# Optimization experiments

Measured on AMD Instinct MI355X. Metric: run time of the kernel, lower is better.

Reference implementation:

```python
import jax, jax.numpy as jnp
import numpy as np

N_NODES = 10000
N_EDGES = 160000
K = 25          # Chebyshev order
H = 12          # temporal filter length == time axis of x
G1 = 32         # conv output channels
NUM_CLASSES = 10
BATCH = 32


def setup_inputs() -> dict:
    key = jax.random.key(0)
    k0, k1, k2, k3 = jax.random.split(key, 4)
    x = jax.random.normal(k0, (BATCH, N_NODES, H), dtype=jnp.float32)
    edge_index = jax.random.randint(k1, (2, N_EDGES), 0, N_NODES, dtype=jnp.int32)
    conv_w = jax.random.normal(k2, (K, H, 1, G1), dtype=jnp.float32) * (1.0 / np.sqrt(K * H))
    conv_b = jnp.zeros((G1,), dtype=jnp.float32)
    fc_w = jax.random.normal(k3, (NUM_CLASSES, N_NODES * G1), dtype=jnp.float32) * 0.01
    fc_b = jnp.zeros((NUM_CLASSES,), dtype=jnp.float32)
    return {"x": x, "edge_index": edge_index, "conv_w": conv_w,
            "conv_b": conv_b, "fc_w": fc_w, "fc_b": fc_b}


def _forward(x, edge_index, conv_w, conv_b, fc_w, fc_b):
    B, N, T = x.shape
    # real part of FFT along time axis (axis=2), as in the torch forward
    xf = jnp.real(jnp.fft.fft(x, axis=2)).astype(x.dtype)  # [B, N, H]

    row, col = edge_index[0], edge_index[1]
    ones = jnp.ones(row.shape, xf.dtype)
    deg = jax.ops.segment_sum(ones, row, num_segments=N)
    dinv = jnp.where(deg > 0, deg ** -0.5, 0.0)
    # rescaled Laplacian (lmax=2): L~ = L - I = -D^{-1/2} A D^{-1/2}
    norm = -dinv[row] * dinv[col]  # [E]

    def prop(z):  # z: [B, N, H] -> L~ z
        msg = z[:, col, :] * norm[None, :, None]                       # [B, E, H]
        agg = jax.ops.segment_sum(msg.swapaxes(0, 1), row,
                                  num_segments=N)                      # [N, B, H]
        return agg.swapaxes(0, 1)                                      # [B, N, H]

    # Chebyshev recursion: Tx_0 = x, Tx_1 = L~ x, Tx_k = 2 L~ Tx_{k-1} - Tx_{k-2}
    tx_prev = xf
    out = jnp.einsum('bnh,hf->bnf', tx_prev, conv_w[0, :, 0, :])
    tx_cur = prop(tx_prev)
    out = out + jnp.einsum('bnh,hf->bnf', tx_cur, conv_w[1, :, 0, :])
    for k in range(2, K):
        tx_next = 2.0 * prop(tx_cur) - tx_prev
        out = out + jnp.einsum('bnh,hf->bnf', tx_next, conv_w[k, :, 0, :])
        tx_prev, tx_cur = tx_cur, tx_next
    out = out + conv_b                                                 # [B, N, G1]

    h = jax.nn.relu(out).reshape(B, -1)                                # [B, N*G1]
    logits = h @ fc_w.T + fc_b                                         # [B, 10]
    return jax.nn.log_softmax(logits, axis=1)


def reference(x, edge_index, conv_w, conv_b, fc_w, fc_b):
    return _forward(x, edge_index, conv_w, conv_b, fc_w, fc_b)
```

## Files before the change

kernel.cpp:

```cpp
#include <hip/hip_runtime.h>
#include <math.h>

#define N_NODES 10000
#define N_EDGES 160000
#define BATCH 32
#define HLEN 12
#define KORD 25
#define G1 32
#define NCLS 10
#define BH 384
#define BG 1024
#define NQ 8
#define QW 48
#define QU 24
#define RU 192
#define FC1_BLOCKS 313
#define EIN_BLOCKS 2500
#define RED1_BLOCKS 10
#define WPK_N (KORD * 192)

typedef unsigned int uint32;
typedef unsigned short ushort16;
typedef __attribute__((ext_vector_type(8))) short short8v;
typedef __attribute__((ext_vector_type(4))) float f32x4;
typedef __attribute__((ext_vector_type(2))) unsigned int uint2v;

struct U3 { uint32 x, y, z; };

__device__ __forceinline__ float bf16lo(uint32 u) { return __uint_as_float(u << 16); }
__device__ __forceinline__ float bf16hi(uint32 u) { return __uint_as_float(u & 0xffff0000u); }
__device__ __forceinline__ uint32 pack_bf16(float a, float b) {
    uint32 ua = __float_as_uint(a), ub = __float_as_uint(b);
    ua = (ua + 0x7fffu + ((ua >> 16) & 1u)) >> 16;
    ub = (ub + 0x7fffu + ((ub >> 16) & 1u)) & 0xffff0000u;
    return ua | ub;
}
__device__ __forceinline__ ushort16 f2bf(float a) {
    uint32 ua = __float_as_uint(a);
    return (ushort16)((ua + 0x7fffu + ((ua >> 16) & 1u)) >> 16);
}

__global__ void deg_kernel(const int* __restrict__ row, int* __restrict__ cnt) {
    int e = blockIdx.x * 256 + threadIdx.x;
    if (e < N_EDGES) atomicAdd(&cnt[row[e]], 1);
}

__global__ void dinv_kernel(const int* __restrict__ cnt, float* __restrict__ dinv) {
    int n = blockIdx.x * 256 + threadIdx.x;
    if (n < N_NODES) {
        int d = cnt[n];
        dinv[n] = (d > 0) ? 1.0f / sqrtf((float)d) : 0.0f;
    }
}

__global__ __launch_bounds__(1024) void scan_kernel(const int* __restrict__ cnt,
                                                    int* __restrict__ rowstart) {
    __shared__ int sums[1024];
    int t = threadIdx.x;
    const int per = 10;
    int base = t * per;
    int s = 0;
    for (int i = 0; i < per; i++) { int idx = base + i; if (idx < N_NODES) s += cnt[idx]; }
    sums[t] = s;
    __syncthreads();
    for (int off = 1; off < 1024; off <<= 1) {
        int v = 0;
        if (t >= off) v = sums[t - off];
        __syncthreads();
        sums[t] += v;
        __syncthreads();
    }
    int run = sums[t] - s;
    for (int i = 0; i < per; i++) {
        int idx = base + i;
        if (idx < N_NODES) { rowstart[idx] = run; run += cnt[idx]; }
    }
    if (t == 1023) rowstart[N_NODES] = run;
}

__global__ void scatter_kernel(const int* __restrict__ row, const int* __restrict__ col,
                               const float* __restrict__ dinv,
                               const int* __restrict__ rowstart, int* __restrict__ cursor,
                               int2* __restrict__ csr_pack) {
    int e = blockIdx.x * 256 + threadIdx.x;
    if (e < N_EDGES) {
        int r = row[e], c = col[e];
        int p = rowstart[r] + atomicAdd(&cursor[r], 1);
        float nrm = -dinv[r] * dinv[c];
        csr_pack[p] = make_int2(c, __float_as_int(nrm));
    }
}

__global__ void wpack_kernel(const float* __restrict__ conv_w, uint32* __restrict__ w_pk) {
    int idx = blockIdx.x * 256 + threadIdx.x;
    if (idx >= WPK_N) return;
    int k = idx / 192;
    int r = idx % 192;
    int g = r >> 6;
    int j2 = (r >> 5) & 1;
    int f = r & 31;
    int h0 = 4 * g + 2 * j2;
    float a = conv_w[(size_t)k * BH + h0 * G1 + f];
    float b = conv_w[(size_t)k * BH + (h0 + 1) * G1 + f];
    w_pk[idx] = pack_bf16(a, b);
}

__global__ __launch_bounds__(256) void fft_full_kernel(const float* __restrict__ x,
                                                       uint32* __restrict__ T0) {
    __shared__ float C[HLEN][HLEN];
    int t = threadIdx.x;
    if (t < HLEN * HLEN) {
        int k = t / HLEN, tt = t % HLEN;
        C[k][tt] = cosf(0.52359877559829887308f * (float)(k * tt));
    }
    __syncthreads();
    int tid = blockIdx.x * 256 + t;
    if (tid >= N_NODES * BATCH) return;
    int n = tid >> 5, b = tid & 31;
    const float* xp = x + (size_t)b * (N_NODES * HLEN) + (size_t)n * HLEN;
    float xr[HLEN];
#pragma unroll
    for (int i = 0; i < HLEN; i++) xr[i] = xp[i];
    float s[HLEN];
#pragma unroll
    for (int k = 0; k < HLEN; k++) {
        float acc = 0.f;
#pragma unroll
        for (int i = 0; i < HLEN; i++) acc += xr[i] * C[k][i];
        s[k] = acc;
    }
    uint32* o = T0 + (size_t)n * RU + b * 6;
#pragma unroll
    for (int j = 0; j < 6; j++) o[j] = pack_bf16(s[2 * j], s[2 * j + 1]);
}

__global__ __launch_bounds__(256) void spmm_full_kernel(
    const uint32* __restrict__ zcur, const uint32* __restrict__ zprev,
    uint32* __restrict__ znext,
    const int* __restrict__ rowstart, const int2* __restrict__ csr_pack,
    float alpha, float beta) {
    int t = threadIdx.x;
    int wv = t >> 6, l = t & 63;
    int node = blockIdx.x * 4 + wv;
    int lo3 = 3 * l;

    float a0 = 0.f, a1 = 0.f, a2 = 0.f, a3 = 0.f, a4 = 0.f, a5 = 0.f;
    int e0 = rowstart[node], e1 = rowstart[node + 1];
    int e = e0;
    if ((e & 1) && e < e1) {
        int2 p = csr_pack[e];
        float nrm = __int_as_float(p.y);
        U3 u = *(const U3*)(zcur + p.x * RU + lo3);
        a0 += nrm * bf16lo(u.x); a1 += nrm * bf16hi(u.x);
        a2 += nrm * bf16lo(u.y); a3 += nrm * bf16hi(u.y);
        a4 += nrm * bf16lo(u.z); a5 += nrm * bf16hi(u.z);
        e++;
    }
    const int4* csr4 = (const int4*)csr_pack;
    int npair = (e1 - e) >> 1;
    int base = e >> 1;
    int nch = npair >> 1;
    if (nch > 0) {
        int4 c0 = csr4[base], c1 = csr4[base + 1];
        for (int ch = 0; ch < nch; ch++) {
            int4 p0 = c0, p1 = c1;
            if (ch + 1 < nch) {
                c0 = csr4[base + 2 * ch + 2];
                c1 = csr4[base + 2 * ch + 3];
            }
            U3 uA = *(const U3*)(zcur + p0.x * RU + lo3);
            U3 uB = *(const U3*)(zcur + p0.z * RU + lo3);
            U3 uC = *(const U3*)(zcur + p1.x * RU + lo3);
            U3 uD = *(const U3*)(zcur + p1.z * RU + lo3);
            float nA = __int_as_float(p0.y), nB = __int_as_float(p0.w);
            float nC = __int_as_float(p1.y), nD = __int_as_float(p1.w);
            a0 += nA * bf16lo(uA.x) + nB * bf16lo(uB.x) + nC * bf16lo(uC.x) + nD * bf16lo(uD.x);
            a1 += nA * bf16hi(uA.x) + nB * bf16hi(uB.x) + nC * bf16hi(uC.x) + nD * bf16hi(uD.x);
            a2 += nA * bf16lo(uA.y) + nB * bf16lo(uB.y) + nC * bf16lo(uC.y) + nD * bf16lo(uD.y);
            a3 += nA * bf16hi(uA.y) + nB * bf16hi(uB.y) + nC * bf16hi(uC.y) + nD * bf16hi(uD.y);
            a4 += nA * bf16lo(uA.z) + nB * bf16lo(uB.z) + nC * bf16lo(uC.z) + nD * bf16lo(uD.z);
            a5 += nA * bf16hi(uA.z) + nB * bf16hi(uB.z) + nC * bf16hi(uC.z) + nD * bf16hi(uD.z);
        }
        e += nch * 4;
    }
    for (; e + 2 <= e1; e += 2) {
        int4 p = csr4[e >> 1];
        U3 uA = *(const U3*)(zcur + p.x * RU + lo3);
        U3 uB = *(const U3*)(zcur + p.z * RU + lo3);
        float nA = __int_as_float(p.y), nB = __int_as_float(p.w);
        a0 += nA * bf16lo(uA.x) + nB * bf16lo(uB.x);
        a1 += nA * bf16hi(uA.x) + nB * bf16hi(uB.x);
        a2 += nA * bf16lo(uA.y) + nB * bf16lo(uB.y);
        a3 += nA * bf16hi(uA.y) + nB * bf16hi(uB.y);
        a4 += nA * bf16lo(uA.z) + nB * bf16lo(uB.z);
        a5 += nA * bf16hi(uA.z) + nB * bf16hi(uB.z);
    }
    if (e < e1) {
        int2 p = csr_pack[e];
        float nrm = __int_as_float(p.y);
        U3 u = *(const U3*)(zcur + p.x * RU + lo3);
        a0 += nrm * bf16lo(u.x); a1 += nrm * bf16hi(u.x);
        a2 += nrm * bf16lo(u.y); a3 += nrm * bf16hi(u.y);
        a4 += nrm * bf16lo(u.z); a5 += nrm * bf16hi(u.z);
    }
    int idx = node * RU + lo3;
    U3 pu = *(const U3*)(zprev + idx);
    U3 ov;
    ov.x = pack_bf16(alpha * a0 - beta * bf16lo(pu.x), alpha * a1 - beta * bf16hi(pu.x));
    ov.y = pack_bf16(alpha * a2 - beta * bf16lo(pu.y), alpha * a3 - beta * bf16hi(pu.y));
    ov.z = pack_bf16(alpha * a4 - beta * bf16lo(pu.z), alpha * a5 - beta * bf16hi(pu.z));
    *(U3*)(znext + idx) = ov;
}

__global__ __launch_bounds__(256) void einfc_mfma_kernel(
    const uint32* __restrict__ T_all,
    const uint32* __restrict__ w_pk,
    const float* __restrict__ conv_b,
    const float* __restrict__ fc_w,
    float* __restrict__ partials) {
    __shared__ float lgacc[BATCH * NCLS];
    int t = threadIdx.x;
    for (int i = t; i < BATCH * NCLS; i += 256) lgacc[i] = 0.f;
    __syncthreads();
    int wv = t >> 6, l = t & 63;
    int node = blockIdx.x * 4 + wv;
    int g = l >> 4;
    int m = l & 15;
    bool gz = (g == 3);

    f32x4 acc00 = {0.f, 0.f, 0.f, 0.f};
    f32x4 acc01 = {0.f, 0.f, 0.f, 0.f};
    f32x4 acc10 = {0.f, 0.f, 0.f, 0.f};
    f32x4 acc11 = {0.f, 0.f, 0.f, 0.f};

    size_t aoff0 = (size_t)m * 6 + 2 * g;
    size_t aoff1 = (size_t)(m + 16) * 6 + 2 * g;

#pragma unroll
    for (int k = 0; k < KORD; k++) {
        const uint32* row = T_all + ((size_t)k * N_NODES + node) * RU;
        uint2v a0 = {0, 0}, a1 = {0, 0};
        uint32 b0u0 = 0, b0u1 = 0, b1u0 = 0, b1u1 = 0;
        if (!gz) {
            a0 = __builtin_nontemporal_load((const uint2v*)(row + aoff0));
            a1 = __builtin_nontemporal_load((const uint2v*)(row + aoff1));
            const uint32* wp = w_pk + (k * 3 + g) * 64 + m;
            b0u0 = wp[0];  b0u1 = wp[32];
            b1u0 = wp[16]; b1u1 = wp[48];
        }
        union { short8v v; uint32 u[4]; } A0, A1, B0, B1;
        A0.u[0] = a0.x; A0.u[1] = a0.y; A0.u[2] = 0; A0.u[3] = 0;
        A1.u[0] = a1.x; A1.u[1] = a1.y; A1.u[2] = 0; A1.u[3] = 0;
        B0.u[0] = b0u0; B0.u[1] = b0u1; B0.u[2] = 0; B0.u[3] = 0;
        B1.u[0] = b1u0; B1.u[1] = b1u1; B1.u[2] = 0; B1.u[3] = 0;
        acc00 = __builtin_amdgcn_mfma_f32_16x16x32_bf16(A0.v, B0.v, acc00, 0, 0, 0);
        acc01 = __builtin_amdgcn_mfma_f32_16x16x32_bf16(A0.v, B1.v, acc01, 0, 0, 0);
        acc10 = __builtin_amdgcn_mfma_f32_16x16x32_bf16(A1.v, B0.v, acc10, 0, 0, 0);
        acc11 = __builtin_amdgcn_mfma_f32_16x16x32_bf16(A1.v, B1.v, acc11, 0, 0, 0);
    }

    float cb0 = conv_b[m];
    float cb1 = conv_b[m + 16];
    float fw0[NCLS], fw1[NCLS];
#pragma unroll
    for (int c = 0; c < NCLS; c++) {
        const float* fp = fc_w + (size_t)c * (N_NODES * G1) + (size_t)node * G1;
        fw0[c] = fp[m];
        fw1[c] = fp[m + 16];
    }
#pragma unroll
    for (int bi = 0; bi < 2; bi++) {
        f32x4 aF = bi ? acc10 : acc00;
        f32x4 aS = bi ? acc11 : acc01;
#pragma unroll
        for (int reg = 0; reg < 4; reg++) {
            float h0 = fmaxf(aF[reg] + cb0, 0.f);
            float h1 = fmaxf(aS[reg] + cb1, 0.f);
            int b = bi * 16 + 4 * g + reg;
#pragma unroll
            for (int c = 0; c < NCLS; c++) {
                float sc = h0 * fw0[c] + h1 * fw1[c];
                sc += __shfl_xor(sc, 1);
                sc += __shfl_xor(sc, 2);
                sc += __shfl_xor(sc, 4);
                sc += __shfl_xor(sc, 8);
                if (m == 0) atomicAdd(&lgacc[b * NCLS + c], sc);
            }
        }
    }
    __syncthreads();
    for (int i = t; i < BATCH * NCLS; i += 256)
        partials[(size_t)blockIdx.x * (BATCH * NCLS) + i] = lgacc[i];
}

__global__ __launch_bounds__(320) void red1_kernel(const float* __restrict__ partials,
                                                   float* __restrict__ red) {
    int t = threadIdx.x;
    int j = blockIdx.x;
    int i0 = j * (EIN_BLOCKS / RED1_BLOCKS);
    int i1 = i0 + (EIN_BLOCKS / RED1_BLOCKS);
    float s0 = 0.f, s1 = 0.f, s2 = 0.f, s3 = 0.f;
    int i = i0;
    for (; i + 4 <= i1; i += 4) {
        s0 += partials[(size_t)(i + 0) * (BATCH * NCLS) + t];
        s1 += partials[(size_t)(i + 1) * (BATCH * NCLS) + t];
        s2 += partials[(size_t)(i + 2) * (BATCH * NCLS) + t];
        s3 += partials[(size_t)(i + 3) * (BATCH * NCLS) + t];
    }
    for (; i < i1; i++) s0 += partials[(size_t)i * (BATCH * NCLS) + t];
    red[(size_t)j * (BATCH * NCLS) + t] = s0 + s1 + s2 + s3;
}

__global__ __launch_bounds__(256) void fft_slice_kernel(const float* __restrict__ x,
                                                        ushort16* __restrict__ xf) {
    __shared__ float C[HLEN][HLEN];
    int t = threadIdx.x;
    if (t < HLEN * HLEN) {
        int k = t / HLEN, tt = t % HLEN;
        C[k][tt] = cosf(0.52359877559829887308f * (float)(k * tt));
    }
    __syncthreads();
    int tid = blockIdx.x * 256 + t;
    if (tid >= N_NODES * BATCH) return;
    int n = tid >> 5, b = tid & 31;
    const float* xp = x + (size_t)b * (N_NODES * HLEN) + (size_t)n * HLEN;
    float xr[HLEN];
#pragma unroll
    for (int i = 0; i < HLEN; i++) xr[i] = xp[i];
    int q = b >> 2, bl = b & 3;
    ushort16* o = xf + ((size_t)q * N_NODES + n) * QW + bl * HLEN;
#pragma unroll
    for (int k = 0; k < HLEN; k++) {
        float s = 0.f;
#pragma unroll
        for (int i = 0; i < HLEN; i++) s += xr[i] * C[k][i];
        o[k] = f2bf(s);
    }
}

__global__ __launch_bounds__(256) void k0_split_kernel(const uint32* __restrict__ z,
                                                       float* __restrict__ out,
                                                       const float* __restrict__ w0) {
    __shared__ float zs[4][QW];
    __shared__ float wk[HLEN * G1];
    int t = threadIdx.x;
    int wv = t >> 6, lane = t & 63;
    int bid = blockIdx.x;
    int q = bid & 7;
    int node = (bid >> 3) * 4 + wv;
    for (int i = t; i < HLEN * G1; i += 256) wk[i] = w0[i];
    if (lane < QU) {
        uint32 u = z[((size_t)q * N_NODES + node) * QU + lane];
        zs[wv][2 * lane]     = bf16lo(u);
        zs[wv][2 * lane + 1] = bf16hi(u);
    }
    __syncthreads();
    float* op = out + (size_t)node * BG + q * 128;
#pragma unroll
    for (int r = 0; r < 2; r++) {
        int j = lane + 64 * r;
        int bl = j >> 5, f = j & 31;
        const float* zb = &zs[wv][bl * HLEN];
        float s = 0.f;
#pragma unroll
        for (int h = 0; h < HLEN; h++) s += zb[h] * wk[h * G1 + f];
        op[j] = s;
    }
}

__global__ __launch_bounds__(256) void spmm_fused_kernel(
    const uint32* __restrict__ zcur, const uint32* __restrict__ zprev,
    uint32* __restrict__ znext, float* __restrict__ out,
    const int* __restrict__ rowstart, const int2* __restrict__ csr_pack,
    const float* __restrict__ wkg, float alpha, float beta) {
    __shared__ float zs[4][QW];
    __shared__ float wk[HLEN * G1];
    int t = threadIdx.x;
    int wv = t >> 6, lane = t & 63;
    int bid = blockIdx.x;
    int q = bid & 7;
    int node = (bid >> 3) * 4 + wv;
    for (int i = t; i < HLEN * G1; i += 256) wk[i] = wkg[i];

    const uint32* zq = zcur + (size_t)q * ((size_t)N_NODES * QU);
    int g  = (lane >= 24) ? 1 : 0;
    int li = lane - g * 24;
    float a0 = 0.f, a1 = 0.f;
    int e0 = rowstart[node], e1 = rowstart[node + 1];
    if (lane < 48) {
        int e = e0;
        if ((e & 1) && e < e1) {
            if (g == 0) {
                int2 p = csr_pack[e];
                float nrm = __int_as_float(p.y);
                uint32 u = zq[p.x * QU + li];
                a0 += nrm * bf16lo(u);
                a1 += nrm * bf16hi(u);
            }
            e++;
        }
        const int4* csr4 = (const int4*)csr_pack;
        int npair = (e1 - e) >> 1;
        int base = e >> 1;
        int nchunk = npair >> 2;
        if (nchunk > 0) {
            int4 c0 = csr4[base];
            int4 c1 = csr4[base + 1];
            int4 c2 = csr4[base + 2];
            int4 c3 = csr4[base + 3];
            for (int ch = 0; ch < nchunk; ch++) {
                int4 p0 = c0, p1 = c1, p2 = c2, p3 = c3;
                if (ch + 1 < nchunk) {
                    int b2 = base + (ch + 1) * 4;
                    c0 = csr4[b2];
                    c1 = csr4[b2 + 1];
                    c2 = csr4[b2 + 2];
                    c3 = csr4[b2 + 3];
                }
                int col0 = g ? p0.z : p0.x;  float n0 = __int_as_float(g ? p0.w : p0.y);
                int col1 = g ? p1.z : p1.x;  float n1 = __int_as_float(g ? p1.w : p1.y);
                int col2 = g ? p2.z : p2.x;  float n2 = __int_as_float(g ? p2.w : p2.y);
                int col3 = g ? p3.z : p3.x;  float n3 = __int_as_float(g ? p3.w : p3.y);
                uint32 u0 = zq[col0 * QU + li];
                uint32 u1 = zq[col1 * QU + li];
                uint32 u2 = zq[col2 * QU + li];
                uint32 u3 = zq[col3 * QU + li];
                a0 += n0 * bf16lo(u0) + n1 * bf16lo(u1);
                a1 += n0 * bf16hi(u0) + n1 * bf16hi(u1);
                a0 += n2 * bf16lo(u2) + n3 * bf16lo(u3);
                a1 += n2 * bf16hi(u2) + n3 * bf16hi(u3);
            }
            e += nchunk * 8;
        }
        for (; e + 2 <= e1; e += 2) {
            int4 p = csr4[e >> 1];
            int col = g ? p.z : p.x;
            float nrm = __int_as_float(g ? p.w : p.y);
            uint32 u = zq[col * QU + li];
            a0 += nrm * bf16lo(u);
            a1 += nrm * bf16hi(u);
        }
        if (e < e1 && g == 0) {
            int2 p = csr_pack[e];
            float nrm = __int_as_float(p.y);
            uint32 u = zq[p.x * QU + li];
            a0 += nrm * bf16lo(u);
            a1 += nrm * bf16hi(u);
        }
    }
    float o0 = __shfl(a0, li + 24);
    float o1 = __shfl(a1, li + 24);
    if (lane < 24) {
        a0 += o0;
        a1 += o1;
        int idx = (q * N_NODES + node) * QU + li;
        uint32 pu = zprev[idx];
        float v0 = alpha * a0 - beta * bf16lo(pu);
        float v1 = alpha * a1 - beta * bf16hi(pu);
        znext[idx] = pack_bf16(v0, v1);
        zs[wv][2 * li]     = v0;
        zs[wv][2 * li + 1] = v1;
    }
    __syncthreads();
    float* op = out + (size_t)node * BG + q * 128;
#pragma unroll
    for (int r = 0; r < 2; r++) {
        int j = lane + 64 * r;
        int bl = j >> 5, f = j & 31;
        const float* zb = &zs[wv][bl * HLEN];
        float s = 0.f;
#pragma unroll
        for (int h = 0; h < HLEN; h++) s += zb[h] * wk[h * G1 + f];
        op[j] += s;
    }
}

__global__ __launch_bounds__(256) void fc1_kernel(const float* __restrict__ out,
                                                  const float* __restrict__ conv_b,
                                                  const float* __restrict__ fc_w,
                                                  float* __restrict__ partials) {
    int t = threadIdx.x;
    int b = t >> 3;
    int sq = t & 7;
    int f0 = sq * 4;
    float4 cb4 = *(const float4*)(conv_b + f0);

    int n0 = blockIdx.x * 32;
    int n1 = n0 + 32;
    if (n1 > N_NODES) n1 = N_NODES;

    float acc[NCLS];
#pragma unroll
    for (int c = 0; c < NCLS; c++) acc[c] = 0.f;

    for (int n = n0; n < n1; n++) {
        float4 o = *(const float4*)(out + (size_t)n * BG + b * G1 + f0);
        o.x += cb4.x; o.y += cb4.y; o.z += cb4.z; o.w += cb4.w;
        o.x = o.x > 0.f ? o.x : 0.f;
        o.y = o.y > 0.f ? o.y : 0.f;
        o.z = o.z > 0.f ? o.z : 0.f;
        o.w = o.w > 0.f ? o.w : 0.f;
        const float* wp = fc_w + (size_t)n * G1 + f0;
#pragma unroll
        for (int c = 0; c < NCLS; c++) {
            float4 w = *(const float4*)(wp + (size_t)c * (N_NODES * G1));
            acc[c] += o.x * w.x + o.y * w.y + o.z * w.z + o.w * w.w;
        }
    }
#pragma unroll
    for (int c = 0; c < NCLS; c++) {
        float v = acc[c];
        v += __shfl_xor(v, 1);
        v += __shfl_xor(v, 2);
        v += __shfl_xor(v, 4);
        if (sq == 0) partials[(size_t)blockIdx.x * (BATCH * NCLS) + b * NCLS + c] = v;
    }
}

__global__ __launch_bounds__(320) void fc2_kernel(const float* __restrict__ partials,
                                                  const float* __restrict__ fc_b,
                                                  float* __restrict__ outp, int nblocks) {
    __shared__ float lg[BATCH][NCLS];
    int t = threadIdx.x;
    int b = t / NCLS, c = t % NCLS;
    float a0 = 0.f, a1 = 0.f, a2 = 0.f, a3 = 0.f;
    int i = 0;
    for (; i + 4 <= nblocks; i += 4) {
        a0 += partials[(size_t)(i + 0) * (BATCH * NCLS) + t];
        a1 += partials[(size_t)(i + 1) * (BATCH * NCLS) + t];
        a2 += partials[(size_t)(i + 2) * (BATCH * NCLS) + t];
        a3 += partials[(size_t)(i + 3) * (BATCH * NCLS) + t];
    }
    for (; i < nblocks; i++) a0 += partials[(size_t)i * (BATCH * NCLS) + t];
    lg[b][c] = a0 + a1 + a2 + a3 + fc_b[c];
    __syncthreads();
    if (t < BATCH) {
        float v[NCLS];
        float m = -1e30f;
#pragma unroll
        for (int cc = 0; cc < NCLS; cc++) { v[cc] = lg[t][cc]; m = fmaxf(m, v[cc]); }
        float s = 0.f;
#pragma unroll
        for (int cc = 0; cc < NCLS; cc++) s += expf(v[cc] - m);
        float ls = logf(s);
#pragma unroll
        for (int cc = 0; cc < NCLS; cc++) outp[t * NCLS + cc] = v[cc] - m - ls;
    }
}

extern "C" void kernel_launch(void* const* d_in, const int* in_sizes, int n_in,
                              void* d_out, int out_size, void* d_ws, size_t ws_size,
                              hipStream_t stream) {
    const float* x      = (const float*)d_in[0];
    const int*   ei     = (const int*)d_in[1];
    const float* conv_w = (const float*)d_in[2];
    const float* conv_b = (const float*)d_in[3];
    const float* fc_w   = (const float*)d_in[4];
    const float* fc_b   = (const float*)d_in[5];
    float* outp = (float*)d_out;

    const int* row = ei;
    const int* col = ei + N_EDGES;

    const size_t SLAB_U = (size_t)N_NODES * RU;

    char* ws = (char*)d_ws;
    size_t off = 0;
    auto alloc = [&](size_t bytes) -> void* {
        void* p = ws + off;
        off = (off + bytes + 255) & ~(size_t)255;
        return p;
    };
    int*    cnt      = (int*)alloc(sizeof(int) * N_NODES);
    float*  dinv     = (float*)alloc(sizeof(float) * N_NODES);
    int*    rowstart = (int*)alloc(sizeof(int) * (N_NODES + 1));
    int*    cursor   = (int*)alloc(sizeof(int) * N_NODES);
    int2*   csr_pack = (int2*)alloc(sizeof(int2) * N_EDGES);
    uint32* w_pk     = (uint32*)alloc(sizeof(uint32) * WPK_N);
    float*  partials = (float*)alloc(sizeof(float) * EIN_BLOCKS * BATCH * NCLS);
    float*  red      = (float*)cnt;

    const size_t T_ALL_BYTES = sizeof(uint32) * SLAB_U * KORD;
    bool big = (ws_size > off && (ws_size - off) >= T_ALL_BYTES + 65536);

    hipMemsetAsync(cnt, 0, sizeof(int) * N_NODES, stream);
    hipMemsetAsync(cursor, 0, sizeof(int) * N_NODES, stream);

    deg_kernel<<<(N_EDGES + 255) / 256, 256, 0, stream>>>(row, cnt);
    dinv_kernel<<<(N_NODES + 255) / 256, 256, 0, stream>>>(cnt, dinv);
    scan_kernel<<<1, 1024, 0, stream>>>(cnt, rowstart);
    scatter_kernel<<<(N_EDGES + 255) / 256, 256, 0, stream>>>(row, col, dinv, rowstart,
                                                              cursor, csr_pack);

    if (big) {
        uint32* T_all = (uint32*)alloc(T_ALL_BYTES);
        wpack_kernel<<<(WPK_N + 255) / 256, 256, 0, stream>>>(conv_w, w_pk);
        fft_full_kernel<<<(N_NODES * BATCH + 255) / 256, 256, 0, stream>>>(x, T_all);
        spmm_full_kernel<<<N_NODES / 4, 256, 0, stream>>>(T_all, T_all, T_all + SLAB_U,
                                                          rowstart, csr_pack, 1.0f, 0.0f);
        for (int k = 2; k < KORD; k++) {
            spmm_full_kernel<<<N_NODES / 4, 256, 0, stream>>>(
                T_all + SLAB_U * (size_t)(k - 1), T_all + SLAB_U * (size_t)(k - 2),
                T_all + SLAB_U * (size_t)k, rowstart, csr_pack, 2.0f, 1.0f);
        }
        einfc_mfma_kernel<<<EIN_BLOCKS, 256, 0, stream>>>(T_all, w_pk, conv_b, fc_w,
                                                          partials);
        red1_kernel<<<RED1_BLOCKS, 320, 0, stream>>>(partials, red);
        fc2_kernel<<<1, 320, 0, stream>>>(red, fc_b, outp, RED1_BLOCKS);
    } else {
        float*  outacc = (float*)alloc(sizeof(float) * (size_t)N_NODES * BG);
        uint32* slabA  = (uint32*)alloc(sizeof(uint32) * SLAB_U);
        uint32* slabB  = (uint32*)alloc(sizeof(uint32) * SLAB_U);
        const int GRID = (N_NODES / 4) * NQ;

        fft_slice_kernel<<<(N_NODES * BATCH + 255) / 256, 256, 0, stream>>>(
            x, (ushort16*)slabA);
        k0_split_kernel<<<GRID, 256, 0, stream>>>(slabA, outacc, conv_w);
        spmm_fused_kernel<<<GRID, 256, 0, stream>>>(slabA, slabA, slabB, outacc,
                                                    rowstart, csr_pack, conv_w + 1 * BH,
                                                    1.0f, 0.0f);
        uint32* zprev = slabA;
        uint32* zcur  = slabB;
        for (int k = 2; k < KORD; k++) {
            spmm_fused_kernel<<<GRID, 256, 0, stream>>>(zcur, zprev, zprev, outacc,
                                                        rowstart, csr_pack,
                                                        conv_w + (size_t)k * BH,
                                                        2.0f, 1.0f);
            uint32* tmp = zprev; zprev = zcur; zcur = tmp;
        }
        fc1_kernel<<<FC1_BLOCKS, 256, 0, stream>>>(outacc, conv_b, fc_w, partials);
        fc2_kernel<<<1, 320, 0, stream>>>(partials, fc_b, outp, FC1_BLOCKS);
    }
}
```

Before: 545.8 us.

## Partition CSR rows by column half and stage conv weights in LDS

```diff
diff --git a/kernel.cpp b/kernel.cpp
--- a/kernel.cpp
+++ b/kernel.cpp
@@ -3,6 +3,7 @@
 
 #define N_NODES 10000
 #define N_EDGES 160000
+#define HALF_N 5000
 #define BATCH 32
 #define HLEN 12
 #define KORD 25
@@ -18,6 +19,9 @@
 #define EIN_BLOCKS 2500
 #define RED1_BLOCKS 10
 #define WPK_N (KORD * 192)
+#define WCHUNKS (KORD * 3)
+#define WSTRIDE 80
+#define WLDS_N (WCHUNKS * WSTRIDE)
 
 typedef unsigned int uint32;
 typedef unsigned short ushort16;
@@ -40,9 +44,13 @@
     return (ushort16)((ua + 0x7fffu + ((ua >> 16) & 1u)) >> 16);
 }
 
-__global__ void deg_kernel(const int* __restrict__ row, int* __restrict__ cnt) {
+__global__ void deg_kernel(const int* __restrict__ row, const int* __restrict__ col,
+                           int* __restrict__ cnt, int* __restrict__ cnt0) {
     int e = blockIdx.x * 256 + threadIdx.x;
-    if (e < N_EDGES) atomicAdd(&cnt[row[e]], 1);
+    if (e < N_EDGES) {
+        atomicAdd(&cnt[row[e]], 1);
+        if (col[e] < HALF_N) atomicAdd(&cnt0[row[e]], 1);
+    }
 }
 
 __global__ void dinv_kernel(const int* __restrict__ cnt, float* __restrict__ dinv) {
@@ -78,14 +86,24 @@
     if (t == 1023) rowstart[N_NODES] = run;
 }
 
+__global__ void rowmid_kernel(const int* __restrict__ rowstart,
+                              const int* __restrict__ cnt0, int* __restrict__ rowmid) {
+    int n = blockIdx.x * 256 + threadIdx.x;
+    if (n < N_NODES) rowmid[n] = rowstart[n] + cnt0[n];
+}
+
 __global__ void scatter_kernel(const int* __restrict__ row, const int* __restrict__ col,
                                const float* __restrict__ dinv,
-                               const int* __restrict__ rowstart, int* __restrict__ cursor,
+                               const int* __restrict__ rowstart,
+                               const int* __restrict__ rowmid,
+                               int* __restrict__ cursor0, int* __restrict__ cursor1,
                                int2* __restrict__ csr_pack) {
     int e = blockIdx.x * 256 + threadIdx.x;
     if (e < N_EDGES) {
         int r = row[e], c = col[e];
-        int p = rowstart[r] + atomicAdd(&cursor[r], 1);
+        int p;
+        if (c < HALF_N) p = rowstart[r] + atomicAdd(&cursor0[r], 1);
+        else            p = rowmid[r]  + atomicAdd(&cursor1[r], 1);
         float nrm = -dinv[r] * dinv[c];
         csr_pack[p] = make_int2(c, __float_as_int(nrm));
     }
@@ -134,19 +152,10 @@
     for (int j = 0; j < 6; j++) o[j] = pack_bf16(s[2 * j], s[2 * j + 1]);
 }
 
-__global__ __launch_bounds__(256) void spmm_full_kernel(
-    const uint32* __restrict__ zcur, const uint32* __restrict__ zprev,
-    uint32* __restrict__ znext,
-    const int* __restrict__ rowstart, const int2* __restrict__ csr_pack,
-    float alpha, float beta) {
-    int t = threadIdx.x;
-    int wv = t >> 6, l = t & 63;
-    int node = blockIdx.x * 4 + wv;
-    int lo3 = 3 * l;
-
-    float a0 = 0.f, a1 = 0.f, a2 = 0.f, a3 = 0.f, a4 = 0.f, a5 = 0.f;
-    int e0 = rowstart[node], e1 = rowstart[node + 1];
-    int e = e0;
+__device__ __forceinline__ void gather_range(
+    const uint32* __restrict__ zcur, const int2* __restrict__ csr_pack,
+    int e, int e1, int lo3,
+    float& a0, float& a1, float& a2, float& a3, float& a4, float& a5) {
     if ((e & 1) && e < e1) {
         int2 p = csr_pack[e];
         float nrm = __int_as_float(p.y);
@@ -203,6 +212,23 @@
         a2 += nrm * bf16lo(u.y); a3 += nrm * bf16hi(u.y);
         a4 += nrm * bf16lo(u.z); a5 += nrm * bf16hi(u.z);
     }
+}
+
+__global__ __launch_bounds__(256) void spmm_full_kernel(
+    const uint32* __restrict__ zcur, const uint32* __restrict__ zprev,
+    uint32* __restrict__ znext,
+    const int* __restrict__ rowstart, const int* __restrict__ rowmid,
+    const int2* __restrict__ csr_pack, float alpha, float beta) {
+    int t = threadIdx.x;
+    int wv = t >> 6, l = t & 63;
+    int node = blockIdx.x * 4 + wv;
+    int lo3 = 3 * l;
+
+    float a0 = 0.f, a1 = 0.f, a2 = 0.f, a3 = 0.f, a4 = 0.f, a5 = 0.f;
+    int e0 = rowstart[node], em = rowmid[node], e1 = rowstart[node + 1];
+    gather_range(zcur, csr_pack, e0, em, lo3, a0, a1, a2, a3, a4, a5);
+    gather_range(zcur, csr_pack, em, e1, lo3, a0, a1, a2, a3, a4, a5);
+
     int idx = node * RU + lo3;
     U3 pu = *(const U3*)(zprev + idx);
     U3 ov;
@@ -219,8 +245,11 @@
     const float* __restrict__ fc_w,
     float* __restrict__ partials) {
     __shared__ float lgacc[BATCH * NCLS];
+    __shared__ uint32 wlds[WLDS_N];
     int t = threadIdx.x;
     for (int i = t; i < BATCH * NCLS; i += 256) lgacc[i] = 0.f;
+    for (int i = t; i < WPK_N; i += 256)
+        wlds[(i >> 6) * WSTRIDE + (i & 63)] = w_pk[i];
     __syncthreads();
     int wv = t >> 6, l = t & 63;
     int node = blockIdx.x * 4 + wv;
@@ -244,7 +273,7 @@
         if (!gz) {
             a0 = __builtin_nontemporal_load((const uint2v*)(row + aoff0));
             a1 = __builtin_nontemporal_load((const uint2v*)(row + aoff1));
-            const uint32* wp = w_pk + (k * 3 + g) * 64 + m;
+            const uint32* wp = wlds + (k * 3 + g) * WSTRIDE + m;
             b0u0 = wp[0];  b0u1 = wp[32];
             b1u0 = wp[16]; b1u1 = wp[48];
         }
@@ -388,59 +417,7 @@
     float a0 = 0.f, a1 = 0.f;
     int e0 = rowstart[node], e1 = rowstart[node + 1];
     if (lane < 48) {
-        int e = e0;
-        if ((e & 1) && e < e1) {
-            if (g == 0) {
-                int2 p = csr_pack[e];
-                float nrm = __int_as_float(p.y);
-                uint32 u = zq[p.x * QU + li];
-                a0 += nrm * bf16lo(u);
-                a1 += nrm * bf16hi(u);
-            }
-            e++;
-        }
-        const int4* csr4 = (const int4*)csr_pack;
-        int npair = (e1 - e) >> 1;
-        int base = e >> 1;
-        int nchunk = npair >> 2;
-        if (nchunk > 0) {
-            int4 c0 = csr4[base];
-            int4 c1 = csr4[base + 1];
-            int4 c2 = csr4[base + 2];
-            int4 c3 = csr4[base + 3];
-            for (int ch = 0; ch < nchunk; ch++) {
-                int4 p0 = c0, p1 = c1, p2 = c2, p3 = c3;
-                if (ch + 1 < nchunk) {
-                    int b2 = base + (ch + 1) * 4;
-                    c0 = csr4[b2];
-                    c1 = csr4[b2 + 1];
-                    c2 = csr4[b2 + 2];
-                    c3 = csr4[b2 + 3];
-                }
-                int col0 = g ? p0.z : p0.x;  float n0 = __int_as_float(g ? p0.w : p0.y);
-                int col1 = g ? p1.z : p1.x;  float n1 = __int_as_float(g ? p1.w : p1.y);
-                int col2 = g ? p2.z : p2.x;  float n2 = __int_as_float(g ? p2.w : p2.y);
-                int col3 = g ? p3.z : p3.x;  float n3 = __int_as_float(g ? p3.w : p3.y);
-                uint32 u0 = zq[col0 * QU + li];
-                uint32 u1 = zq[col1 * QU + li];
-                uint32 u2 = zq[col2 * QU + li];
-                uint32 u3 = zq[col3 * QU + li];
-                a0 += n0 * bf16lo(u0) + n1 * bf16lo(u1);
-                a1 += n0 * bf16hi(u0) + n1 * bf16hi(u1);
-                a0 += n2 * bf16lo(u2) + n3 * bf16lo(u3);
-                a1 += n2 * bf16hi(u2) + n3 * bf16hi(u3);
-            }
-            e += nchunk * 8;
-        }
-        for (; e + 2 <= e1; e += 2) {
-            int4 p = csr4[e >> 1];
-            int col = g ? p.z : p.x;
-            float nrm = __int_as_float(g ? p.w : p.y);
-            uint32 u = zq[col * QU + li];
-            a0 += nrm * bf16lo(u);
-            a1 += nrm * bf16hi(u);
-        }
-        if (e < e1 && g == 0) {
+        for (int e = e0 + g; e < e1; e += 2) {
             int2 p = csr_pack[e];
             float nrm = __int_as_float(p.y);
             uint32 u = zq[p.x * QU + li];
@@ -572,9 +549,12 @@
         return p;
     };
     int*    cnt      = (int*)alloc(sizeof(int) * N_NODES);
+    int*    cnt0     = (int*)alloc(sizeof(int) * N_NODES);
     float*  dinv     = (float*)alloc(sizeof(float) * N_NODES);
     int*    rowstart = (int*)alloc(sizeof(int) * (N_NODES + 1));
-    int*    cursor   = (int*)alloc(sizeof(int) * N_NODES);
+    int*    rowmid   = (int*)alloc(sizeof(int) * N_NODES);
+    int*    cursor0  = (int*)alloc(sizeof(int) * N_NODES);
+    int*    cursor1  = (int*)alloc(sizeof(int) * N_NODES);
     int2*   csr_pack = (int2*)alloc(sizeof(int2) * N_EDGES);
     uint32* w_pk     = (uint32*)alloc(sizeof(uint32) * WPK_N);
     float*  partials = (float*)alloc(sizeof(float) * EIN_BLOCKS * BATCH * NCLS);
@@ -584,24 +564,28 @@
     bool big = (ws_size > off && (ws_size - off) >= T_ALL_BYTES + 65536);
 
     hipMemsetAsync(cnt, 0, sizeof(int) * N_NODES, stream);
-    hipMemsetAsync(cursor, 0, sizeof(int) * N_NODES, stream);
-
-    deg_kernel<<<(N_EDGES + 255) / 256, 256, 0, stream>>>(row, cnt);
+    hipMemsetAsync(cnt0, 0, sizeof(int) * N_NODES, stream);
+    hipMemsetAsync(cursor0, 0, sizeof(int) * N_NODES, stream);
+    hipMemsetAsync(cursor1, 0, sizeof(int) * N_NODES, stream);
+
+    deg_kernel<<<(N_EDGES + 255) / 256, 256, 0, stream>>>(row, col, cnt, cnt0);
     dinv_kernel<<<(N_NODES + 255) / 256, 256, 0, stream>>>(cnt, dinv);
     scan_kernel<<<1, 1024, 0, stream>>>(cnt, rowstart);
-    scatter_kernel<<<(N_EDGES + 255) / 256, 256, 0, stream>>>(row, col, dinv, rowstart,
-                                                              cursor, csr_pack);
+    rowmid_kernel<<<(N_NODES + 255) / 256, 256, 0, stream>>>(rowstart, cnt0, rowmid);
+    scatter_kernel<<<(N_EDGES + 255) / 256, 256, 0, stream>>>(
+        row, col, dinv, rowstart, rowmid, cursor0, cursor1, csr_pack);
 
     if (big) {
         uint32* T_all = (uint32*)alloc(T_ALL_BYTES);
         wpack_kernel<<<(WPK_N + 255) / 256, 256, 0, stream>>>(conv_w, w_pk);
         fft_full_kernel<<<(N_NODES * BATCH + 255) / 256, 256, 0, stream>>>(x, T_all);
         spmm_full_kernel<<<N_NODES / 4, 256, 0, stream>>>(T_all, T_all, T_all + SLAB_U,
-                                                          rowstart, csr_pack, 1.0f, 0.0f);
+                                                          rowstart, rowmid, csr_pack,
+                                                          1.0f, 0.0f);
         for (int k = 2; k < KORD; k++) {
             spmm_full_kernel<<<N_NODES / 4, 256, 0, stream>>>(
                 T_all + SLAB_U * (size_t)(k - 1), T_all + SLAB_U * (size_t)(k - 2),
-                T_all + SLAB_U * (size_t)k, rowstart, csr_pack, 2.0f, 1.0f);
+                T_all + SLAB_U * (size_t)k, rowstart, rowmid, csr_pack, 2.0f, 1.0f);
         }
         einfc_mfma_kernel<<<EIN_BLOCKS, 256, 0, stream>>>(T_all, w_pk, conv_b, fc_w,
                                                           partials);
```

New measurement: 572.1 us. 4.8% more time.
